# Performance work log

Measured on AMD Instinct MI355X. Metric: run time of the kernel, lower is better.

The kernel has to match this reference:

```python
import jax, jax.numpy as jnp
import numpy as np

N = 100000        # nodes
E_HALF = 800000   # random edges before symmetrization
HID = 128         # hidden_dim
K = 4             # Chebyshev order
NEG = 0.01        # leaky_relu negative slope
BN_EPS = 1e-5
L2_EPS = 1e-12


def setup_inputs() -> dict:
    key = jax.random.key(0)
    ks = jax.random.split(key, 4)
    x = jax.random.normal(ks[0], (N, 3), dtype=jnp.float32)
    e = jax.random.randint(ks[1], (2, E_HALF), 0, N, dtype=jnp.int32)
    # symmetrize so the sym-normalized Laplacian is well defined
    edge_index = jnp.concatenate([e, e[::-1]], axis=1).astype(jnp.int64)

    def wcheb(k, fin, fout):
        return jax.random.normal(k, (K, fin, fout), dtype=jnp.float32) * np.float32(1.0 / np.sqrt(fin * K))

    wk = jax.random.split(ks[2], 5)
    return {
        "x": x, "edge_index": edge_index,
        "W1": wcheb(wk[0], 3, HID),   "b1": jnp.zeros((HID,), jnp.float32),
        "W2": wcheb(wk[1], HID, HID), "b2": jnp.zeros((HID,), jnp.float32),
        "W3": wcheb(wk[2], HID, HID), "b3": jnp.zeros((HID,), jnp.float32),
        "W4": wcheb(wk[3], HID, HID), "b4": jnp.zeros((HID,), jnp.float32),
        "g1": jnp.ones((HID,), jnp.float32), "be1": jnp.zeros((HID,), jnp.float32),
        "g2": jnp.ones((HID,), jnp.float32), "be2": jnp.zeros((HID,), jnp.float32),
        "g3": jnp.ones((HID,), jnp.float32), "be3": jnp.zeros((HID,), jnp.float32),
        "Wrep": jax.random.normal(wk[4], (HID, 3), dtype=jnp.float32) * np.float32(1.0 / np.sqrt(HID)),
        "brep": jnp.zeros((3,), jnp.float32),
    }


def _cheb(x, src, dst, norm, W, b):
    """PyG ChebConv (sym norm, lambda_max=2): out = sum_k T_k(L_hat) x @ W_k + b."""
    def prop(t):  # (L_hat t)_i = sum_{e: src->dst==i} norm_e * t[src_e]
        return jax.ops.segment_sum(t[src] * norm[:, None], dst, num_segments=N)
    Tx0 = x
    out = Tx0 @ W[0]
    Tx1 = prop(Tx0)
    out = out + Tx1 @ W[1]
    for k in range(2, W.shape[0]):
        Tx2 = 2.0 * prop(Tx1) - Tx0
        out = out + Tx2 @ W[k]
        Tx0, Tx1 = Tx1, Tx2
    return out + b


def _bn(x, g, b):  # BatchNorm1d, training mode (batch stats, biased var)
    mu = x.mean(axis=0)
    var = ((x - mu) ** 2).mean(axis=0)
    return (x - mu) * jax.lax.rsqrt(var + BN_EPS) * g + b


def _leaky(x):
    return jnp.where(x >= 0, x, NEG * x)


def reference(x, edge_index, W1, b1, W2, b2, W3, b3, W4, b4,
              g1, be1, g2, be2, g3, be3, Wrep, brep):
    src, dst = edge_index[0], edge_index[1]
    deg = jax.ops.segment_sum(jnp.ones(src.shape, jnp.float32), src, num_segments=N)
    dinv = jnp.where(deg > 0, jax.lax.rsqrt(jnp.maximum(deg, 1.0)), 0.0)
    # scaled Laplacian L_hat = -D^{-1/2} A D^{-1/2} (zero diagonal) for lambda_max=2
    norm = -(dinv[src] * dinv[dst])  # [E]

    h = _cheb(x.astype(jnp.float32), src, dst, norm, W1, b1)
    h = _bn(_leaky(h), g1, be1)
    h = _cheb(h, src, dst, norm, W2, b2)
    h = _bn(_leaky(h), g2, be2)
    h = _cheb(h, src, dst, norm, W3, b3)
    h = _bn(jnp.maximum(h, 0.0), g3, be3)
    h = _cheb(h, src, dst, norm, W4, b4)
    h = h / jnp.maximum(jnp.linalg.norm(h, axis=1, keepdims=True), L2_EPS)
    return h @ Wrep + brep  # [N, 3]
```

## Files before the change

kernel.cpp:

```cpp
#include <hip/hip_runtime.h>
#include <hip/hip_bf16.h>


#define HID 128
#define NEG 0.01f
#define BN_EPS 1e-5f
#define L2_EPS 1e-12f
#define CAP 64

typedef __attribute__((ext_vector_type(8))) short short8;
typedef __attribute__((ext_vector_type(4))) float floatx4;

__device__ __forceinline__ short f2bf(float f) {
    unsigned u = __float_as_uint(f);
    return (short)((u + 0x7fffu + ((u >> 16) & 1u)) >> 16);
}
__device__ __forceinline__ unsigned pack2bf(float x, float y) {
    return (unsigned)(unsigned short)f2bf(x) | ((unsigned)(unsigned short)f2bf(y) << 16);
}
__device__ __forceinline__ float bflo(unsigned u) { return __uint_as_float(u << 16); }
__device__ __forceinline__ float bfhi(unsigned u) { return __uint_as_float(u & 0xffff0000u); }
__device__ __forceinline__ float bf2f(unsigned short h) { return __uint_as_float((unsigned)h << 16); }

__device__ __forceinline__ float actf(float v, int act) {
    if (act == 0) return v >= 0.f ? v : NEG * v;
    if (act == 1) return v > 0.f ? v : 0.f;
    return v;
}


__global__ __launch_bounds__(256) void k_zero(int* __restrict__ arr, float* __restrict__ S, int N) {
    int i = blockIdx.x * 256 + threadIdx.x;
    if (i < N) arr[i * CAP] = 0;
    if (blockIdx.x == 0) {
        for (int k = threadIdx.x; k < 1024; k += 256) S[k] = 0.f;
    }
}

__global__ __launch_bounds__(256) void k_fillpad(const int* __restrict__ src, const int* __restrict__ dst,
                                                 int* __restrict__ arr, int E) {
    int e = blockIdx.x * 256 + threadIdx.x;
    if (e >= E) return;
    int d = dst[e];
    int pos = atomicAdd(&arr[d * CAP], 1);
    if (pos < CAP - 1) arr[d * CAP + 1 + pos] = src[e];
}

__global__ __launch_bounds__(256) void k_dinv(const int* __restrict__ arr, float* __restrict__ dinv,
                                              int* __restrict__ cnt, int N) {
    int i = blockIdx.x * 256 + threadIdx.x;
    if (i < N) {
        int d = arr[i * CAP];
        dinv[i] = d > 0 ? rsqrtf((float)d) : 0.f;
        cnt[i] = d < CAP - 1 ? d : CAP - 1;
    }
}

__global__ __launch_bounds__(256) void k_norm(const int* __restrict__ arr, const int* __restrict__ cnt,
                                              const float* __restrict__ dinv, int2* __restrict__ edges,
                                              float* __restrict__ snorm, int N) {
    int node = blockIdx.x * 4 + (threadIdx.x >> 6);
    if (node >= N) return;
    node = __builtin_amdgcn_readfirstlane(node);
    int lane = threadIdx.x & 63;
    int deg = cnt[node];
    float dd = dinv[node];
    int s = (lane < deg) ? arr[node * CAP + 1 + lane] : 0;
    float w = (lane < deg) ? -(dinv[s] * dd) : 0.f;
    if (lane < deg) {
        int2 rec;
        rec.x = s;
        rec.y = __float_as_int(w);
        edges[node * CAP + lane] = rec;
    }
    float sw = w;
    #pragma unroll
    for (int d = 1; d < 64; d <<= 1) sw += __shfl_xor(sw, d);
    if (lane == 0) snorm[node] = sw;
}


__global__ __launch_bounds__(256) void k_prop3(const float* __restrict__ T, const float* __restrict__ prev,
                                               float* __restrict__ out, const int* __restrict__ cnt,
                                               const int2* __restrict__ edges,
                                               float a, float b, int N) {
    int i = blockIdx.x * 256 + threadIdx.x;
    if (i >= N) return;
    float a0 = 0.f, a1 = 0.f, a2 = 0.f;
    int deg = cnt[i];
    int base = i * CAP;
    for (int j = 0; j < deg; ++j) {
        int2 r = edges[base + j];
        float w = __int_as_float(r.y);
        a0 += w * T[r.x * 3 + 0];
        a1 += w * T[r.x * 3 + 1];
        a2 += w * T[r.x * 3 + 2];
    }
    float r0 = a * a0, r1 = a * a1, r2 = a * a2;
    if (prev) {
        r0 += b * prev[i * 3 + 0];
        r1 += b * prev[i * 3 + 1];
        r2 += b * prev[i * 3 + 2];
    }
    out[i * 3 + 0] = r0;
    out[i * 3 + 1] = r1;
    out[i * 3 + 2] = r2;
}

__global__ __launch_bounds__(256) void k_prop1(const unsigned* __restrict__ OUT,
                                               unsigned* __restrict__ T1, unsigned* __restrict__ T0,
                                               const int* __restrict__ cnt, const int2* __restrict__ edges,
                                               const float* __restrict__ snorm, const float* __restrict__ S,
                                               const float* __restrict__ g, const float* __restrict__ be,
                                               int act, float invN, int N) {
    int node = blockIdx.x * 4 + (threadIdx.x >> 6);
    if (node >= N) return;
    node = __builtin_amdgcn_readfirstlane(node);
    int lane = threadIdx.x & 63;
    int f0 = 2 * lane;
    float mu0 = S[f0] * invN, mu1 = S[f0 + 1] * invN;
    float v0 = S[f0 + 128] * invN - mu0 * mu0;
    float v1 = S[f0 + 129] * invN - mu1 * mu1;
    float a0 = g[f0] * rsqrtf(v0 + BN_EPS), a1 = g[f0 + 1] * rsqrtf(v1 + BN_EPS);
    float c0 = be[f0] - mu0 * a0, c1 = be[f0 + 1] - mu1 * a1;

    int deg = cnt[node];
    const int2* eb = edges + (size_t)node * CAP;
    float accx = 0.f, accy = 0.f;
    int j = 0;
    int nb = deg >> 3;
    if (nb > 0) {
        int2 recA[8]; unsigned tA[8];
        int2 recB[8]; unsigned tB[8];
        #pragma unroll
        for (int k = 0; k < 8; ++k) recA[k] = eb[k];
        #pragma unroll
        for (int k = 0; k < 8; ++k) tA[k] = OUT[(size_t)recA[k].x * 64 + lane];
        for (int bi = 1; bi < nb; ++bi) {
            const int2* ebb = eb + bi * 8;
            #pragma unroll
            for (int k = 0; k < 8; ++k) recB[k] = ebb[k];
            #pragma unroll
            for (int k = 0; k < 8; ++k) tB[k] = OUT[(size_t)recB[k].x * 64 + lane];
            #pragma unroll
            for (int k = 0; k < 8; ++k) {
                float w = __int_as_float(recA[k].y);
                accx += w * actf(bflo(tA[k]), act);
                accy += w * actf(bfhi(tA[k]), act);
            }
            #pragma unroll
            for (int k = 0; k < 8; ++k) { recA[k] = recB[k]; tA[k] = tB[k]; }
        }
        #pragma unroll
        for (int k = 0; k < 8; ++k) {
            float w = __int_as_float(recA[k].y);
            accx += w * actf(bflo(tA[k]), act);
            accy += w * actf(bfhi(tA[k]), act);
        }
        j = nb * 8;
    }
    for (; j < deg; ++j) {
        int2 r = eb[j];
        float w = __int_as_float(r.y);
        unsigned t0 = OUT[(size_t)r.x * 64 + lane];
        accx += w * actf(bflo(t0), act);
        accy += w * actf(bfhi(t0), act);
    }
    float si = snorm[node];
    __builtin_nontemporal_store(pack2bf(a0 * accx + si * c0, a1 * accy + si * c1),
                                &T1[(size_t)node * 64 + lane]);
    unsigned h = OUT[(size_t)node * 64 + lane];
    float t0lo = a0 * actf(bflo(h), act) + c0;
    float t0hi = a1 * actf(bfhi(h), act) + c1;
    __builtin_nontemporal_store(pack2bf(t0lo, t0hi), &T0[(size_t)node * 64 + lane]);
}

__global__ __launch_bounds__(256) void k_prop128(const unsigned* __restrict__ T, const unsigned* __restrict__ prev,
                                                 unsigned* __restrict__ out, const int* __restrict__ cnt,
                                                 const int2* __restrict__ edges,
                                                 float a, float b, int N) {
    int node = blockIdx.x * 4 + (threadIdx.x >> 6);
    if (node >= N) return;
    node = __builtin_amdgcn_readfirstlane(node);
    int lane = threadIdx.x & 63;
    int deg = cnt[node];
    const int2* eb = edges + (size_t)node * CAP;
    float accx = 0.f, accy = 0.f;
    int j = 0;
    int nb = deg >> 3;
    if (nb > 0) {
        int2 recA[8]; unsigned tA[8];
        int2 recB[8]; unsigned tB[8];
        #pragma unroll
        for (int k = 0; k < 8; ++k) recA[k] = eb[k];
        #pragma unroll
        for (int k = 0; k < 8; ++k) tA[k] = T[(size_t)recA[k].x * 64 + lane];
        for (int bi = 1; bi < nb; ++bi) {
            const int2* ebb = eb + bi * 8;
            #pragma unroll
            for (int k = 0; k < 8; ++k) recB[k] = ebb[k];
            #pragma unroll
            for (int k = 0; k < 8; ++k) tB[k] = T[(size_t)recB[k].x * 64 + lane];
            #pragma unroll
            for (int k = 0; k < 8; ++k) {
                float w = __int_as_float(recA[k].y);
                accx += w * bflo(tA[k]);
                accy += w * bfhi(tA[k]);
            }
            #pragma unroll
            for (int k = 0; k < 8; ++k) { recA[k] = recB[k]; tA[k] = tB[k]; }
        }
        #pragma unroll
        for (int k = 0; k < 8; ++k) {
            float w = __int_as_float(recA[k].y);
            accx += w * bflo(tA[k]);
            accy += w * bfhi(tA[k]);
        }
        j = nb * 8;
    }
    for (; j < deg; ++j) {
        int2 r = eb[j];
        float w = __int_as_float(r.y);
        unsigned t0 = T[(size_t)r.x * 64 + lane];
        accx += w * bflo(t0);
        accy += w * bfhi(t0);
    }
    float rx = a * accx, ry = a * accy;
    if (prev) {
        unsigned p = __builtin_nontemporal_load(&prev[(size_t)node * 64 + lane]);
        rx += b * bflo(p);
        ry += b * bfhi(p);
    }
    __builtin_nontemporal_store(pack2bf(rx, ry), &out[(size_t)node * 64 + lane]);
}


__global__ __launch_bounds__(256) void k_gemm1(const float* __restrict__ x, const float* __restrict__ t1,
                                               const float* __restrict__ t2, const float* __restrict__ t3,
                                               const float* __restrict__ W, const float* __restrict__ b,
                                               unsigned short* __restrict__ OUT, float* __restrict__ S,
                                               int npb, int N) {
    __shared__ float Wl[12 * 128];
    __shared__ float bl[128];
    __shared__ float sS[256];
    int tid = threadIdx.x;
    for (int i = tid; i < 1536; i += 256) Wl[i] = W[i];
    if (tid < 128) bl[tid] = b[tid];
    if (tid < 256) sS[tid] = 0.f;
    __syncthreads();
    int f = tid & 127;
    int base = blockIdx.x * npb;
    int end = base + npb < N ? base + npb : N;
    const float* rows[4] = {x, t1, t2, t3};
    float s1 = 0.f, s2 = 0.f;
    for (int node = base + (tid >> 7); node < end; node += 2) {
        float acc = bl[f];
        #pragma unroll
        for (int k = 0; k < 4; ++k) {
            const float* r = rows[k] + (size_t)node * 3;
            acc += r[0] * Wl[(k * 3 + 0) * 128 + f];
            acc += r[1] * Wl[(k * 3 + 1) * 128 + f];
            acc += r[2] * Wl[(k * 3 + 2) * 128 + f];
        }
        unsigned short h = (unsigned short)f2bf(acc);
        OUT[(size_t)node * 128 + f] = h;
        float u = actf(bf2f(h), 0);
        s1 += u;
        s2 += u * u;
    }
    atomicAdd(&sS[f], s1);
    atomicAdd(&sS[f + 128], s2);
    __syncthreads();
    if (tid < 256) atomicAdd(&S[tid], sS[tid]);
}


__global__ __launch_bounds__(256) void k_packW(const float* __restrict__ WA, const float* __restrict__ WB,
                                               const float* __restrict__ WC, short* __restrict__ Wp) {
    int gid = blockIdx.x * 256 + threadIdx.x;
    int L = gid >> 16;
    int idx = gid & 65535;
    int j = idx & 7;
    int lane = (idx >> 3) & 63;
    int rest = idx >> 9;
    int nt = rest & 7;
    int ks = rest >> 3;
    int kk = ks * 32 + (lane >> 4) * 8 + j;
    int c = nt * 16 + (lane & 15);
    const float* W = (L == 0) ? WA : (L == 1) ? WB : WC;
    Wp[gid] = f2bf(W[(size_t)(kk >> 7) * 16384 + (kk & 127) * 128 + c]);
}

__global__ __launch_bounds__(512) void k_gemm512(const short* __restrict__ T0, const short* __restrict__ T1,
                                                 const short* __restrict__ T2, const short* __restrict__ T3,
                                                 const short* __restrict__ Wp, const float* __restrict__ bias,
                                                 unsigned short* __restrict__ OUT, float* __restrict__ S,
                                                 const float* __restrict__ Wrep, const float* __restrict__ brep,
                                                 float* __restrict__ fout,
                                                 int M, int doStats, int doFinal, int act) {
    __shared__ short Wlds[65536];
    __shared__ float sS[256];
    __shared__ float sW[388];
    int tid = threadIdx.x;
    int lane = tid & 63, wave = tid >> 6;
    if (tid < 256) sS[tid] = 0.f;
    if (doFinal) {
        for (int i = tid; i < 384; i += 512) sW[i] = Wrep[i];
        if (tid < 3) sW[384 + tid] = brep[tid];
    }
    for (int i = tid; i < 8192; i += 512) ((int4*)Wlds)[i] = ((const int4*)Wp)[i];
    __syncthreads();

    int quad = lane >> 4;
    int col0 = lane & 15;
    const short* Ts[4] = {T0, T1, T2, T3};
    float s1[8], s2[8];
    #pragma unroll
    for (int i = 0; i < 8; ++i) { s1[i] = 0.f; s2[i] = 0.f; }

    int nt32 = (M + 31) / 32;
    int stride = gridDim.x * 8;
    for (int t = blockIdx.x * 8 + wave; t < nt32; t += stride) {
        int r0 = t * 32;
        int rowa = r0 + col0;
        int rowb = rowa + 16;
        size_t rb0 = (size_t)(rowa < M ? rowa : M - 1) * 128;
        size_t rb1 = (size_t)(rowb < M ? rowb : M - 1) * 128;
        floatx4 acc0[8], acc1[8];
        #pragma unroll
        for (int i = 0; i < 8; ++i) {
            acc0[i][0] = 0.f; acc0[i][1] = 0.f; acc0[i][2] = 0.f; acc0[i][3] = 0.f;
            acc1[i][0] = 0.f; acc1[i][1] = 0.f; acc1[i][2] = 0.f; acc1[i][3] = 0.f;
        }
        #pragma unroll 4
        for (int ks = 0; ks < 16; ++ks) {
            const short* Tm = Ts[ks >> 2];
            int aoff = (ks & 3) * 32 + quad * 8;
            short8 af0 = *((const short8*)(Tm + rb0 + aoff));
            short8 af1 = *((const short8*)(Tm + rb1 + aoff));
            #pragma unroll
            for (int nt = 0; nt < 8; ++nt) {
                short8 bf = *((const short8*)(Wlds + ((ks * 8 + nt) * 64 + lane) * 8));
                acc0[nt] = __builtin_amdgcn_mfma_f32_16x16x32_bf16(af0, bf, acc0[nt], 0, 0, 0);
                acc1[nt] = __builtin_amdgcn_mfma_f32_16x16x32_bf16(af1, bf, acc1[nt], 0, 0, 0);
            }
        }
        if (doFinal) {
            #pragma unroll
            for (int half = 0; half < 2; ++half) {
                #pragma unroll
                for (int rg = 0; rg < 4; ++rg) {
                    int r = r0 + half * 16 + quad * 4 + rg;
                    float sq = 0.f, p0 = 0.f, p1 = 0.f, p2 = 0.f;
                    #pragma unroll
                    for (int nt = 0; nt < 8; ++nt) {
                        int c = nt * 16 + col0;
                        float v = (half ? acc1[nt][rg] : acc0[nt][rg]) + bias[c];
                        sq += v * v;
                        p0 += v * sW[c * 3 + 0];
                        p1 += v * sW[c * 3 + 1];
                        p2 += v * sW[c * 3 + 2];
                    }
                    #pragma unroll
                    for (int d = 1; d < 16; d <<= 1) {
                        sq += __shfl_xor(sq, d);
                        p0 += __shfl_xor(p0, d);
                        p1 += __shfl_xor(p1, d);
                        p2 += __shfl_xor(p2, d);
                    }
                    if (col0 == 0 && r < M) {
                        float inv = 1.f / fmaxf(sqrtf(sq), L2_EPS);
                        fout[r * 3 + 0] = p0 * inv + sW[384];
                        fout[r * 3 + 1] = p1 * inv + sW[385];
                        fout[r * 3 + 2] = p2 * inv + sW[386];
                    }
                }
            }
        } else {
            #pragma unroll
            for (int half = 0; half < 2; ++half) {
                int rbase = r0 + half * 16 + quad * 4;
                #pragma unroll
                for (int nt = 0; nt < 8; ++nt) {
                    int c = nt * 16 + col0;
                    float bv = bias[c];
                    #pragma unroll
                    for (int rg = 0; rg < 4; ++rg) {
                        int r = rbase + rg;
                        if (r < M) {
                            float v = (half ? acc1[nt][rg] : acc0[nt][rg]) + bv;
                            unsigned short h = (unsigned short)f2bf(v);
                            OUT[(size_t)r * 128 + c] = h;
                            float u = actf(bf2f(h), act);
                            s1[nt] += u;
                            s2[nt] += u * u;
                        }
                    }
                }
            }
        }
    }
    if (doStats) {
        #pragma unroll
        for (int nt = 0; nt < 8; ++nt) {
            int c = nt * 16 + col0;
            atomicAdd(&sS[c], s1[nt]);
            atomicAdd(&sS[c + 128], s2[nt]);
        }
        __syncthreads();
        if (tid < 256) atomicAdd(&S[tid], sS[tid]);
    }
}


extern "C" void kernel_launch(void* const* d_in, const int* in_sizes, int n_in,
                              void* d_out, int out_size, void* d_ws, size_t ws_size,
                              hipStream_t stream) {
    const int N = in_sizes[0] / 3;
    const int E = in_sizes[1] / 2;

    const float* x    = (const float*)d_in[0];
    const int*   ei   = (const int*)d_in[1];
    const int* esrc = ei;
    const int* edst = ei + E;
    const float* W1 = (const float*)d_in[2];  const float* b1 = (const float*)d_in[3];
    const float* W2 = (const float*)d_in[4];  const float* b2 = (const float*)d_in[5];
    const float* W3 = (const float*)d_in[6];  const float* b3 = (const float*)d_in[7];
    const float* W4 = (const float*)d_in[8];  const float* b4 = (const float*)d_in[9];
    const float* g1 = (const float*)d_in[10]; const float* be1 = (const float*)d_in[11];
    const float* g2 = (const float*)d_in[12]; const float* be2 = (const float*)d_in[13];
    const float* g3 = (const float*)d_in[14]; const float* be3 = (const float*)d_in[15];
    const float* Wrep = (const float*)d_in[16]; const float* brep = (const float*)d_in[17];
    float* out = (float*)d_out;

    char* w = (char*)d_ws;
    size_t off = 0;
    auto alloc = [&](size_t bytes) { size_t o = off; off = (off + bytes + 255) & ~(size_t)255; return o; };
    int*   arr    = (int*)(w + alloc((size_t)N * CAP * 4));
    int*   cnt    = (int*)(w + alloc((size_t)N * 4));
    float* dinv   = (float*)(w + alloc((size_t)N * 4));
    float* snorm  = (float*)(w + alloc((size_t)N * 4));
    int2*  edges  = (int2*)(w + alloc((size_t)N * CAP * 8));
    short* Wp     = (short*)(w + alloc(3 * 65536 * 2));
    float* S      = (float*)(w + alloc(4 * 256 * 4));
    float* t1f    = (float*)(w + alloc((size_t)N * 3 * 4));
    float* t2f    = (float*)(w + alloc((size_t)N * 3 * 4));
    float* t3f    = (float*)(w + alloc((size_t)N * 3 * 4));
    short* T0     = (short*)(w + alloc((size_t)N * 128 * 2));
    short* T1     = (short*)(w + alloc((size_t)N * 128 * 2));
    short* T2     = (short*)(w + alloc((size_t)N * 128 * 2));
    short* T3     = (short*)(w + alloc((size_t)N * 128 * 2));
    unsigned short* OUT = (unsigned short*)(w + alloc((size_t)N * 128 * 2));

    int gE = (E + 255) / 256;
    int gN = (N + 255) / 256;
    int gW = (N + 3) / 4;
    float invN = 1.f / (float)N;
    int npb = (N + 255) / 256;

    k_zero<<<gN, 256, 0, stream>>>(arr, S, N);
    k_fillpad<<<gE, 256, 0, stream>>>(esrc, edst, arr, E);
    k_dinv<<<gN, 256, 0, stream>>>(arr, dinv, cnt, N);
    k_norm<<<gW, 256, 0, stream>>>(arr, cnt, dinv, edges, snorm, N);
    k_packW<<<768, 256, 0, stream>>>(W2, W3, W4, Wp);

    k_prop3<<<gN, 256, 0, stream>>>(x, nullptr, t1f, cnt, edges, 1.f, 0.f, N);
    k_prop3<<<gN, 256, 0, stream>>>(t1f, x, t2f, cnt, edges, 2.f, -1.f, N);
    k_prop3<<<gN, 256, 0, stream>>>(t2f, t1f, t3f, cnt, edges, 2.f, -1.f, N);
    k_gemm1<<<256, 256, 0, stream>>>(x, t1f, t2f, t3f, W1, b1, OUT, S, npb, N);

    const float* bs[3]  = {b2, b3, b4};
    const float* gs[3]  = {g2, g3, nullptr};
    const float* bes[3] = {be2, be3, nullptr};
    int actsIn[3] = {0, 0, 1};
    int actsOut[3] = {0, 1, 2};

    for (int l = 0; l < 3; ++l) {
        float* Sin = S + (size_t)l * 256;
        float* Sout = S + (size_t)(l + 1) * 256;
        const float* gc = (l == 0) ? g1 : gs[l - 1];
        const float* bc = (l == 0) ? be1 : bes[l - 1];
        k_prop1<<<gW, 256, 0, stream>>>((const unsigned*)OUT, (unsigned*)T1, (unsigned*)T0,
                                        cnt, edges, snorm, Sin, gc, bc, actsIn[l], invN, N);
        k_prop128<<<gW, 256, 0, stream>>>((const unsigned*)T1, (const unsigned*)T0, (unsigned*)T2,
                                          cnt, edges, 2.f, -1.f, N);
        k_prop128<<<gW, 256, 0, stream>>>((const unsigned*)T2, (const unsigned*)T1, (unsigned*)T3,
                                          cnt, edges, 2.f, -1.f, N);
        k_gemm512<<<256, 512, 0, stream>>>(T0, T1, T2, T3, Wp + (size_t)l * 65536, bs[l], OUT, Sout,
                                           Wrep, brep, out, N,
                                           l < 2 ? 1 : 0, l == 2 ? 1 : 0, actsOut[l]);
    }
}
```

Measured before the change: 1.080 ms.

## Slice feature layout into 16-column panels and gather per slice

Stores the hidden activations in a sliced layout, with 8 panels of 16 bf16 columns, each panel contiguous over nodes. Propagation kernels now launch 8 blocks per node group, one per slice, and each wave gathers 8 edges at a time with 8 lanes per edge before reducing across lanes with shuffles. The goal is a smaller working set per slice so neighbour gathers hit cache better. The cost is re-reading the edge lists 8 times and 32-byte gathers per edge. The GEMM and first-layer kernels are updated to read and write the new layout, and edge padding slots are now written with zero weights so the blocked loop can read past the degree.

```diff
diff --git a/kernel.cpp b/kernel.cpp
--- a/kernel.cpp
+++ b/kernel.cpp
@@ -67,12 +67,10 @@
     float dd = dinv[node];
     int s = (lane < deg) ? arr[node * CAP + 1 + lane] : 0;
     float w = (lane < deg) ? -(dinv[s] * dd) : 0.f;
-    if (lane < deg) {
-        int2 rec;
-        rec.x = s;
-        rec.y = __float_as_int(w);
-        edges[node * CAP + lane] = rec;
-    }
+    int2 rec;
+    rec.x = s;
+    rec.y = __float_as_int(w);
+    edges[node * CAP + lane] = rec;
     float sw = w;
     #pragma unroll
     for (int d = 1; d < 64; d <<= 1) sw += __shfl_xor(sw, d);
@@ -107,131 +105,84 @@
     out[i * 3 + 2] = r2;
 }
 
+__global__ __launch_bounds__(256) void k_prop128(const unsigned* __restrict__ T, const unsigned* __restrict__ prev,
+                                                 unsigned* __restrict__ out, const int* __restrict__ cnt,
+                                                 const int2* __restrict__ edges,
+                                                 float a, float b, int N) {
+    int slice = blockIdx.x & 7;
+    int node = (blockIdx.x >> 3) * 4 + (threadIdx.x >> 6);
+    if (node >= N) return;
+    node = __builtin_amdgcn_readfirstlane(node);
+    int lane = threadIdx.x & 63;
+    int g = lane >> 3, u = lane & 7;
+    int deg = cnt[node];
+    const int2* eb = edges + (size_t)node * CAP;
+    const unsigned* Ts = T + (size_t)slice * N * 8;
+    float accx = 0.f, accy = 0.f;
+    int nb = (deg + 7) >> 3;
+    for (int bi = 0; bi < nb; ++bi) {
+        int2 rec = eb[bi * 8 + g];
+        unsigned t = Ts[(size_t)rec.x * 8 + u];
+        float w = __int_as_float(rec.y);
+        accx += w * bflo(t);
+        accy += w * bfhi(t);
+    }
+    accx += __shfl_xor(accx, 8); accx += __shfl_xor(accx, 16); accx += __shfl_xor(accx, 32);
+    accy += __shfl_xor(accy, 8); accy += __shfl_xor(accy, 16); accy += __shfl_xor(accy, 32);
+    if (g == 0) {
+        size_t o = (size_t)slice * N * 8 + (size_t)node * 8 + u;
+        float rx = a * accx, ry = a * accy;
+        if (prev) {
+            unsigned p = prev[o];
+            rx += b * bflo(p);
+            ry += b * bfhi(p);
+        }
+        out[o] = pack2bf(rx, ry);
+    }
+}
+
 __global__ __launch_bounds__(256) void k_prop1(const unsigned* __restrict__ OUT,
                                                unsigned* __restrict__ T1, unsigned* __restrict__ T0,
                                                const int* __restrict__ cnt, const int2* __restrict__ edges,
                                                const float* __restrict__ snorm, const float* __restrict__ S,
-                                               const float* __restrict__ g, const float* __restrict__ be,
+                                               const float* __restrict__ g_, const float* __restrict__ be,
                                                int act, float invN, int N) {
-    int node = blockIdx.x * 4 + (threadIdx.x >> 6);
+    int slice = blockIdx.x & 7;
+    int node = (blockIdx.x >> 3) * 4 + (threadIdx.x >> 6);
     if (node >= N) return;
     node = __builtin_amdgcn_readfirstlane(node);
     int lane = threadIdx.x & 63;
-    int f0 = 2 * lane;
+    int g = lane >> 3, u = lane & 7;
+    int f0 = slice * 16 + 2 * u;
     float mu0 = S[f0] * invN, mu1 = S[f0 + 1] * invN;
     float v0 = S[f0 + 128] * invN - mu0 * mu0;
     float v1 = S[f0 + 129] * invN - mu1 * mu1;
-    float a0 = g[f0] * rsqrtf(v0 + BN_EPS), a1 = g[f0 + 1] * rsqrtf(v1 + BN_EPS);
+    float a0 = g_[f0] * rsqrtf(v0 + BN_EPS), a1 = g_[f0 + 1] * rsqrtf(v1 + BN_EPS);
     float c0 = be[f0] - mu0 * a0, c1 = be[f0 + 1] - mu1 * a1;
 
     int deg = cnt[node];
     const int2* eb = edges + (size_t)node * CAP;
+    const unsigned* Os = OUT + (size_t)slice * N * 8;
     float accx = 0.f, accy = 0.f;
-    int j = 0;
-    int nb = deg >> 3;
-    if (nb > 0) {
-        int2 recA[8]; unsigned tA[8];
-        int2 recB[8]; unsigned tB[8];
-        #pragma unroll
-        for (int k = 0; k < 8; ++k) recA[k] = eb[k];
-        #pragma unroll
-        for (int k = 0; k < 8; ++k) tA[k] = OUT[(size_t)recA[k].x * 64 + lane];
-        for (int bi = 1; bi < nb; ++bi) {
-            const int2* ebb = eb + bi * 8;
-            #pragma unroll
-            for (int k = 0; k < 8; ++k) recB[k] = ebb[k];
-            #pragma unroll
-            for (int k = 0; k < 8; ++k) tB[k] = OUT[(size_t)recB[k].x * 64 + lane];
-            #pragma unroll
-            for (int k = 0; k < 8; ++k) {
-                float w = __int_as_float(recA[k].y);
-                accx += w * actf(bflo(tA[k]), act);
-                accy += w * actf(bfhi(tA[k]), act);
-            }
-            #pragma unroll
-            for (int k = 0; k < 8; ++k) { recA[k] = recB[k]; tA[k] = tB[k]; }
-        }
-        #pragma unroll
-        for (int k = 0; k < 8; ++k) {
-            float w = __int_as_float(recA[k].y);
-            accx += w * actf(bflo(tA[k]), act);
-            accy += w * actf(bfhi(tA[k]), act);
-        }
-        j = nb * 8;
-    }
-    for (; j < deg; ++j) {
-        int2 r = eb[j];
-        float w = __int_as_float(r.y);
-        unsigned t0 = OUT[(size_t)r.x * 64 + lane];
-        accx += w * actf(bflo(t0), act);
-        accy += w * actf(bfhi(t0), act);
-    }
-    float si = snorm[node];
-    __builtin_nontemporal_store(pack2bf(a0 * accx + si * c0, a1 * accy + si * c1),
-                                &T1[(size_t)node * 64 + lane]);
-    unsigned h = OUT[(size_t)node * 64 + lane];
-    float t0lo = a0 * actf(bflo(h), act) + c0;
-    float t0hi = a1 * actf(bfhi(h), act) + c1;
-    __builtin_nontemporal_store(pack2bf(t0lo, t0hi), &T0[(size_t)node * 64 + lane]);
-}
-
-__global__ __launch_bounds__(256) void k_prop128(const unsigned* __restrict__ T, const unsigned* __restrict__ prev,
-                                                 unsigned* __restrict__ out, const int* __restrict__ cnt,
-                                                 const int2* __restrict__ edges,
-                                                 float a, float b, int N) {
-    int node = blockIdx.x * 4 + (threadIdx.x >> 6);
-    if (node >= N) return;
-    node = __builtin_amdgcn_readfirstlane(node);
-    int lane = threadIdx.x & 63;
-    int deg = cnt[node];
-    const int2* eb = edges + (size_t)node * CAP;
-    float accx = 0.f, accy = 0.f;
-    int j = 0;
-    int nb = deg >> 3;
-    if (nb > 0) {
-        int2 recA[8]; unsigned tA[8];
-        int2 recB[8]; unsigned tB[8];
-        #pragma unroll
-        for (int k = 0; k < 8; ++k) recA[k] = eb[k];
-        #pragma unroll
-        for (int k = 0; k < 8; ++k) tA[k] = T[(size_t)recA[k].x * 64 + lane];
-        for (int bi = 1; bi < nb; ++bi) {
-            const int2* ebb = eb + bi * 8;
-            #pragma unroll
-            for (int k = 0; k < 8; ++k) recB[k] = ebb[k];
-            #pragma unroll
-            for (int k = 0; k < 8; ++k) tB[k] = T[(size_t)recB[k].x * 64 + lane];
-            #pragma unroll
-            for (int k = 0; k < 8; ++k) {
-                float w = __int_as_float(recA[k].y);
-                accx += w * bflo(tA[k]);
-                accy += w * bfhi(tA[k]);
-            }
-            #pragma unroll
-            for (int k = 0; k < 8; ++k) { recA[k] = recB[k]; tA[k] = tB[k]; }
-        }
-        #pragma unroll
-        for (int k = 0; k < 8; ++k) {
-            float w = __int_as_float(recA[k].y);
-            accx += w * bflo(tA[k]);
-            accy += w * bfhi(tA[k]);
-        }
-        j = nb * 8;
-    }
-    for (; j < deg; ++j) {
-        int2 r = eb[j];
-        float w = __int_as_float(r.y);
-        unsigned t0 = T[(size_t)r.x * 64 + lane];
-        accx += w * bflo(t0);
-        accy += w * bfhi(t0);
-    }
-    float rx = a * accx, ry = a * accy;
-    if (prev) {
-        unsigned p = __builtin_nontemporal_load(&prev[(size_t)node * 64 + lane]);
-        rx += b * bflo(p);
-        ry += b * bfhi(p);
-    }
-    __builtin_nontemporal_store(pack2bf(rx, ry), &out[(size_t)node * 64 + lane]);
+    int nb = (deg + 7) >> 3;
+    for (int bi = 0; bi < nb; ++bi) {
+        int2 rec = eb[bi * 8 + g];
+        unsigned t = Os[(size_t)rec.x * 8 + u];
+        float w = __int_as_float(rec.y);
+        accx += w * actf(bflo(t), act);
+        accy += w * actf(bfhi(t), act);
+    }
+    accx += __shfl_xor(accx, 8); accx += __shfl_xor(accx, 16); accx += __shfl_xor(accx, 32);
+    accy += __shfl_xor(accy, 8); accy += __shfl_xor(accy, 16); accy += __shfl_xor(accy, 32);
+    size_t o = (size_t)slice * N * 8 + (size_t)node * 8 + u;
+    if (g == 0) {
+        float si = snorm[node];
+        T1[o] = pack2bf(a0 * accx + si * c0, a1 * accy + si * c1);
+    }
+    if (g == 1) {
+        unsigned h = Os[(size_t)node * 8 + u];
+        T0[o] = pack2bf(a0 * actf(bflo(h), act) + c0, a1 * actf(bfhi(h), act) + c1);
+    }
 }
 
 
@@ -249,6 +200,7 @@
     if (tid < 256) sS[tid] = 0.f;
     __syncthreads();
     int f = tid & 127;
+    size_t sb = ((size_t)(f >> 4) * N) * 16 + (f & 15);
     int base = blockIdx.x * npb;
     int end = base + npb < N ? base + npb : N;
     const float* rows[4] = {x, t1, t2, t3};
@@ -263,7 +215,7 @@
             acc += r[2] * Wl[(k * 3 + 2) * 128 + f];
         }
         unsigned short h = (unsigned short)f2bf(acc);
-        OUT[(size_t)node * 128 + f] = h;
+        OUT[sb + (size_t)node * 16] = h;
         float u = actf(bf2f(h), 0);
         s1 += u;
         s2 += u * u;
@@ -324,8 +276,8 @@
         int r0 = t * 32;
         int rowa = r0 + col0;
         int rowb = rowa + 16;
-        size_t rb0 = (size_t)(rowa < M ? rowa : M - 1) * 128;
-        size_t rb1 = (size_t)(rowb < M ? rowb : M - 1) * 128;
+        int ra = rowa < M ? rowa : M - 1;
+        int rb = rowb < M ? rowb : M - 1;
         floatx4 acc0[8], acc1[8];
         #pragma unroll
         for (int i = 0; i < 8; ++i) {
@@ -335,9 +287,10 @@
         #pragma unroll 4
         for (int ks = 0; ks < 16; ++ks) {
             const short* Tm = Ts[ks >> 2];
-            int aoff = (ks & 3) * 32 + quad * 8;
-            short8 af0 = *((const short8*)(Tm + rb0 + aoff));
-            short8 af1 = *((const short8*)(Tm + rb1 + aoff));
+            int f0 = (ks & 3) * 32 + quad * 8;
+            size_t sbase = (size_t)(f0 >> 4) * M * 16 + (f0 & 15);
+            short8 af0 = *((const short8*)(Tm + sbase + (size_t)ra * 16));
+            short8 af1 = *((const short8*)(Tm + sbase + (size_t)rb * 16));
             #pragma unroll
             for (int nt = 0; nt < 8; ++nt) {
                 short8 bf = *((const short8*)(Wlds + ((ks * 8 + nt) * 64 + lane) * 8));
@@ -384,13 +337,14 @@
                 for (int nt = 0; nt < 8; ++nt) {
                     int c = nt * 16 + col0;
                     float bv = bias[c];
+                    size_t sb = (size_t)nt * M * 16 + col0;
                     #pragma unroll
                     for (int rg = 0; rg < 4; ++rg) {
                         int r = rbase + rg;
                         if (r < M) {
                             float v = (half ? acc1[nt][rg] : acc0[nt][rg]) + bv;
                             unsigned short h = (unsigned short)f2bf(v);
-                            OUT[(size_t)r * 128 + c] = h;
+                            OUT[sb + (size_t)r * 16] = h;
                             float u = actf(bf2f(h), act);
                             s1[nt] += u;
                             s2[nt] += u * u;
@@ -455,6 +409,7 @@
     int gE = (E + 255) / 256;
     int gN = (N + 255) / 256;
     int gW = (N + 3) / 4;
+    int gP = 8 * gW;
     float invN = 1.f / (float)N;
     int npb = (N + 255) / 256;
 
@@ -480,11 +435,11 @@
         float* Sout = S + (size_t)(l + 1) * 256;
         const float* gc = (l == 0) ? g1 : gs[l - 1];
         const float* bc = (l == 0) ? be1 : bes[l - 1];
-        k_prop1<<<gW, 256, 0, stream>>>((const unsigned*)OUT, (unsigned*)T1, (unsigned*)T0,
+        k_prop1<<<gP, 256, 0, stream>>>((const unsigned*)OUT, (unsigned*)T1, (unsigned*)T0,
                                         cnt, edges, snorm, Sin, gc, bc, actsIn[l], invN, N);
-        k_prop128<<<gW, 256, 0, stream>>>((const unsigned*)T1, (const unsigned*)T0, (unsigned*)T2,
+        k_prop128<<<gP, 256, 0, stream>>>((const unsigned*)T1, (const unsigned*)T0, (unsigned*)T2,
                                           cnt, edges, 2.f, -1.f, N);
-        k_prop128<<<gW, 256, 0, stream>>>((const unsigned*)T2, (const unsigned*)T1, (unsigned*)T3,
+        k_prop128<<<gP, 256, 0, stream>>>((const unsigned*)T2, (const unsigned*)T1, (unsigned*)T3,
                                           cnt, edges, 2.f, -1.f, N);
         k_gemm512<<<256, 512, 0, stream>>>(T0, T1, T2, T3, Wp + (size_t)l * 65536, bs[l], OUT, Sout,
                                            Wrep, brep, out, N,
```

Result: slower. 2.879 ms (+166.7%).
